# Performance work log

Measured on AMD Instinct MI355X. Metric: run time of the kernel, lower is better.

## Reference

```python
import jax, jax.numpy as jnp
import numpy as np

REG1 = 0.05
REG2 = 0.05

N, D, P = 262144, 256, 512


def setup_inputs() -> dict:
    key = jax.random.key(0)
    kz, kp = jax.random.split(key)
    z = jax.random.normal(kz, (N, D), dtype=jnp.float32)
    # nn.Parameter(torch.rand(P, D)) -> uniform [0, 1)
    prototype_vectors = jax.random.uniform(kp, (P, D), dtype=jnp.float32)
    return {"z": z, "prototype_vectors": prototype_vectors}


def _cdist(a, b):
    # Euclidean pairwise distances [Na, Nb] via the norm trick (matches torch.cdist p=2).
    a2 = jnp.sum(a * a, axis=-1, keepdims=True)          # [Na, 1]
    b2 = jnp.sum(b * b, axis=-1)[None, :]                # [1, Nb]
    sq = a2 + b2 - 2.0 * (a @ b.T)
    return jnp.sqrt(jnp.maximum(sq, 0.0))


def reference(z, prototype_vectors):
    p_dist = _cdist(z, prototype_vectors)                # [N, P]
    f_dist = _cdist(prototype_vectors, z)                # [P, N]
    return (REG1 * jnp.mean(jnp.min(p_dist, axis=1))
            + REG2 * jnp.mean(jnp.min(f_dist, axis=1)))
```

## Files before the change

### kernel.cpp

```cpp
#include <hip/hip_runtime.h>
#include <hip/hip_bf16.h>

#define N_ROWS 262144
#define DDIM   256
#define PROTO  512
#define BM     64
#define RTG    4096
#define NBLK   8192

typedef __bf16 bf16x8 __attribute__((ext_vector_type(8)));
typedef float  f32x4  __attribute__((ext_vector_type(4)));

__global__ void prep_proto(const float* __restrict__ Pm,
                           unsigned short* __restrict__ PBf,
                           float* __restrict__ P2) {
  int p = blockIdx.x;
  int k = threadIdx.x;
  float v = Pm[p * DDIM + k];
  int idx = (p >> 4) * 4096 + (k >> 5) * 512 + ((((k >> 3) & 3) * 16) + (p & 15)) * 8 + (k & 7);
  ((__bf16*)PBf)[idx] = (__bf16)v;
  float sq = v * v;
  #pragma unroll
  for (int m = 1; m < 64; m <<= 1) sq += __shfl_xor(sq, m);
  __shared__ float ws4[4];
  if ((k & 63) == 0) ws4[k >> 6] = sq;
  __syncthreads();
  if (k == 0) P2[p] = (ws4[0] + ws4[1]) + (ws4[2] + ws4[3]);
}

__global__ __launch_bounds__(256, 4)
void proto_main(const float* __restrict__ Z, const unsigned short* __restrict__ PBf,
                const float* __restrict__ P2, float* __restrict__ colpart,
                float* __restrict__ rowminpart) {
  __shared__ __align__(16) unsigned short A_lds[BM * 256];
  __shared__ float z2s[BM];
  __shared__ float rowred[BM * 4];

  const int t   = threadIdx.x;
  const int w   = t >> 6;
  const int l   = t & 63;
  const int l15 = l & 15;
  const int lg  = l >> 4;

  const int bid = blockIdx.x;
  const int g   = ((bid >> 4) << 3) | (bid & 7);
  const int cc  = (bid >> 3) & 1;
  const size_t row0 = (size_t)g * BM;

  const int srow = t >> 2;
  const int sc4  = t & 3;
  {
    const float4* Zv = (const float4*)Z + (row0 + srow) * (DDIM / 4);
    float zacc = 0.f;
    #pragma unroll
    for (int m = 0; m < 8; ++m) {
      float4 a0 = Zv[(sc4 + m * 4) * 2];
      float4 a1 = Zv[(sc4 + m * 4) * 2 + 1];
      zacc += a0.x*a0.x + a0.y*a0.y + a0.z*a0.z + a0.w*a0.w
            + a1.x*a1.x + a1.y*a1.y + a1.z*a1.z + a1.w*a1.w;
      bf16x8 pk;
      pk[0] = (__bf16)a0.x; pk[1] = (__bf16)a0.y; pk[2] = (__bf16)a0.z; pk[3] = (__bf16)a0.w;
      pk[4] = (__bf16)a1.x; pk[5] = (__bf16)a1.y; pk[6] = (__bf16)a1.z; pk[7] = (__bf16)a1.w;
      int slot = (sc4 + m * 4) ^ (srow & 7);
      *(bf16x8*)&A_lds[srow * 256 + slot * 8] = pk;
    }
    zacc += __shfl_xor(zacc, 1);
    zacc += __shfl_xor(zacc, 2);
    if (sc4 == 0) z2s[srow] = zacc;
  }

  float p2r[4];
  #pragma unroll
  for (int j = 0; j < 4; ++j) p2r[j] = P2[cc * 256 + w * 64 + j * 16 + l15];

  __syncthreads();

  f32x4 acc[4][4];
  #pragma unroll
  for (int i = 0; i < 4; ++i)
    #pragma unroll
    for (int j = 0; j < 4; ++j)
      acc[i][j] = (f32x4){0.f, 0.f, 0.f, 0.f};

  const unsigned short* PBw = PBf + (size_t)(cc * 16 + w * 4) * 8 * 512 + l * 8;
  bf16x8 bgn[4];
  #pragma unroll
  for (int j = 0; j < 4; ++j)
    bgn[j] = *(const bf16x8*)&PBw[(size_t)(j * 8) * 512];
  #pragma unroll
  for (int ks = 0; ks < 8; ++ks) {
    bf16x8 bgc[4];
    #pragma unroll
    for (int j = 0; j < 4; ++j) bgc[j] = bgn[j];
    if (ks < 7) {
      #pragma unroll
      for (int j = 0; j < 4; ++j)
        bgn[j] = *(const bf16x8*)&PBw[(size_t)(j * 8 + ks + 1) * 512];
    }
    __builtin_amdgcn_s_setprio(1);
    #pragma unroll
    for (int i = 0; i < 4; ++i) {
      int arow = i * 16 + l15;
      bf16x8 af = *(const bf16x8*)&A_lds[arow * 256 + (((ks * 4 + lg) ^ (l15 & 7)) * 8)];
      #pragma unroll
      for (int j = 0; j < 4; ++j)
        acc[i][j] = __builtin_amdgcn_mfma_f32_16x16x32_bf16(af, bgc[j], acc[i][j], 0, 0, 0);
    }
    __builtin_amdgcn_s_setprio(0);
  }

  float cmin[4] = {3.4e38f, 3.4e38f, 3.4e38f, 3.4e38f};
  #pragma unroll
  for (int i = 0; i < 4; ++i) {
    #pragma unroll
    for (int r = 0; r < 4; ++r) {
      int arow = i * 16 + lg * 4 + r;
      float z2 = z2s[arow];
      float m = 3.4e38f;
      #pragma unroll
      for (int j = 0; j < 4; ++j) {
        float sq = fmaxf(z2 + p2r[j] - 2.0f * acc[i][j][r], 0.0f);
        m = fminf(m, sq);
        cmin[j] = fminf(cmin[j], sq);
      }
      m = fminf(m, __shfl_xor(m, 1));
      m = fminf(m, __shfl_xor(m, 2));
      m = fminf(m, __shfl_xor(m, 4));
      m = fminf(m, __shfl_xor(m, 8));
      if (l15 == 0) rowred[arow * 4 + w] = m;
    }
  }
  #pragma unroll
  for (int j = 0; j < 4; ++j) {
    float c = cmin[j];
    c = fminf(c, __shfl_xor(c, 16));
    c = fminf(c, __shfl_xor(c, 32));
    cmin[j] = c;
  }
  if (l < 16) {
    #pragma unroll
    for (int j = 0; j < 4; ++j)
      colpart[(size_t)g * PROTO + cc * 256 + w * 64 + j * 16 + l] = cmin[j];
  }
  __syncthreads();
  if (t < 64) {
    float m = fminf(fminf(rowred[t * 4], rowred[t * 4 + 1]),
                    fminf(rowred[t * 4 + 2], rowred[t * 4 + 3]));
    rowminpart[(size_t)cc * N_ROWS + row0 + t] = m;
  }
}

__global__ void col_reduce(const float* __restrict__ colpart, float* __restrict__ colfin) {
  int t    = threadIdx.x;
  int colb = blockIdx.x * 16;
  int cl   = t & 15;
  int gg   = t >> 4;
  float m = 3.4e38f;
  for (int g = gg; g < RTG; g += 32)
    m = fminf(m, colpart[(size_t)g * PROTO + colb + cl]);
  m = fminf(m, __shfl_xor(m, 16));
  m = fminf(m, __shfl_xor(m, 32));
  __shared__ float red[8][16];
  if ((t & 63) < 16) red[t >> 6][cl] = m;
  __syncthreads();
  if (t < 16) {
    float r = red[0][t];
    #pragma unroll
    for (int wv = 1; wv < 8; ++wv) r = fminf(r, red[wv][t]);
    colfin[colb + t] = sqrtf(r);
  }
}

__global__ void row_reduce(const float* __restrict__ rowminpart, float* __restrict__ rowsum) {
  int t = threadIdx.x;
  size_t grow = (size_t)blockIdx.x * 256 + t;
  float m = fminf(rowminpart[grow], rowminpart[N_ROWS + grow]);
  float s = sqrtf(m);
  #pragma unroll
  for (int mm = 1; mm < 64; mm <<= 1) s += __shfl_xor(s, mm);
  __shared__ float ws4[4];
  if ((t & 63) == 0) ws4[t >> 6] = s;
  __syncthreads();
  if (t == 0) rowsum[blockIdx.x] = (ws4[0] + ws4[1]) + (ws4[2] + ws4[3]);
}

__global__ void final_reduce(const float* __restrict__ colfin,
                             const float* __restrict__ rowsum,
                             float* __restrict__ out) {
  int t = threadIdx.x;
  float sc = colfin[t];
  float sr = rowsum[t] + rowsum[t + 512];
  #pragma unroll
  for (int mm = 1; mm < 64; mm <<= 1) { sc += __shfl_xor(sc, mm); sr += __shfl_xor(sr, mm); }
  __shared__ float wc[8], wr[8];
  if ((t & 63) == 0) { wc[t >> 6] = sc; wr[t >> 6] = sr; }
  __syncthreads();
  if (t == 0) {
    float tc = 0.f, tr = 0.f;
    #pragma unroll
    for (int i = 0; i < 8; ++i) { tc += wc[i]; tr += wr[i]; }
    out[0] = 0.05f * (tr / (float)N_ROWS) + 0.05f * (tc / (float)PROTO);
  }
}

extern "C" void kernel_launch(void* const* d_in, const int* in_sizes, int n_in,
                              void* d_out, int out_size, void* d_ws, size_t ws_size,
                              hipStream_t stream) {
  const float* z  = (const float*)d_in[0];
  const float* pv = (const float*)d_in[1];
  char* ws = (char*)d_ws;
  size_t off = 0;
  unsigned short* PBf = (unsigned short*)(ws + off); off += 262144;
  float* P2           = (float*)(ws + off);          off += 2048;
  float* colpart      = (float*)(ws + off);          off += (size_t)RTG * PROTO * 4;
  float* colfin       = (float*)(ws + off);          off += 2048;
  float* rowminpart   = (float*)(ws + off);          off += (size_t)2 * N_ROWS * 4;
  float* rowsum       = (float*)(ws + off);          off += 4096;

  prep_proto<<<PROTO, DDIM, 0, stream>>>(pv, PBf, P2);
  proto_main<<<NBLK, 256, 0, stream>>>(z, PBf, P2, colpart, rowminpart);
  col_reduce<<<32, 512, 0, stream>>>(colpart, colfin);
  row_reduce<<<N_ROWS / 256, 256, 0, stream>>>(rowminpart, rowsum);
  final_reduce<<<1, PROTO, 0, stream>>>(colfin, rowsum, (float*)d_out);
}
```

Baseline: 142.2 us.

## Make proto_main persistent over 8 row tiles with double-buffered Z staging

Each block now handles 8 consecutive 64-row tiles instead of one, reducing the grid from 8192 to 1024 blocks. The next tile's Z is prefetched into registers during the current MFMA loop and written to an alternate LDS buffer, and column minima accumulate across tiles. This shrinks the colpart partial array and the col_reduce work. In exchange it doubles LDS use, holds 16 float4 prefetch registers, and lowers the occupancy hint from 4 to 2 blocks per CU.

```diff
diff --git a/kernel.cpp b/kernel.cpp
--- a/kernel.cpp
+++ b/kernel.cpp
@@ -5,8 +5,9 @@
 #define DDIM   256
 #define PROTO  512
 #define BM     64
-#define RTG    4096
-#define NBLK   8192
+#define TPB    8
+#define RGS    512
+#define NBLK   1024
 
 typedef __bf16 bf16x8 __attribute__((ext_vector_type(8)));
 typedef float  f32x4  __attribute__((ext_vector_type(4)));
@@ -28,12 +29,13 @@
   if (k == 0) P2[p] = (ws4[0] + ws4[1]) + (ws4[2] + ws4[3]);
 }
 
-__global__ __launch_bounds__(256, 4)
+__global__ __launch_bounds__(256, 2)
 void proto_main(const float* __restrict__ Z, const unsigned short* __restrict__ PBf,
                 const float* __restrict__ P2, float* __restrict__ colpart,
                 float* __restrict__ rowminpart) {
-  __shared__ __align__(16) unsigned short A_lds[BM * 256];
-  __shared__ float z2s[BM];
+  __shared__ __align__(16) unsigned short A0[BM * 256];
+  __shared__ __align__(16) unsigned short A1[BM * 256];
+  __shared__ float z2s[2][BM];
   __shared__ float rowred[BM * 4];
 
   const int t   = threadIdx.x;
@@ -43,110 +45,145 @@
   const int lg  = l >> 4;
 
   const int bid = blockIdx.x;
-  const int g   = ((bid >> 4) << 3) | (bid & 7);
+  const int rg  = ((bid >> 4) << 3) | (bid & 7);
   const int cc  = (bid >> 3) & 1;
-  const size_t row0 = (size_t)g * BM;
 
   const int srow = t >> 2;
   const int sc4  = t & 3;
+
+  float p2r[4];
+  #pragma unroll
+  for (int j = 0; j < 4; ++j) p2r[j] = P2[cc * 256 + w * 64 + j * 16 + l15];
+
+  float colmin[4] = {3.4e38f, 3.4e38f, 3.4e38f, 3.4e38f};
+
+  const unsigned short* PBw = PBf + (size_t)(cc * 16 + w * 4) * 4096 + l * 8;
+
+  float4 za[16];
   {
-    const float4* Zv = (const float4*)Z + (row0 + srow) * (DDIM / 4);
+    const float4* Zv = (const float4*)Z + ((size_t)rg * TPB * BM + srow) * (DDIM / 4);
+    #pragma unroll
+    for (int m = 0; m < 8; ++m) {
+      za[2 * m]     = Zv[(sc4 + m * 4) * 2];
+      za[2 * m + 1] = Zv[(sc4 + m * 4) * 2 + 1];
+    }
     float zacc = 0.f;
     #pragma unroll
     for (int m = 0; m < 8; ++m) {
-      float4 a0 = Zv[(sc4 + m * 4) * 2];
-      float4 a1 = Zv[(sc4 + m * 4) * 2 + 1];
+      float4 a0 = za[2 * m], a1 = za[2 * m + 1];
       zacc += a0.x*a0.x + a0.y*a0.y + a0.z*a0.z + a0.w*a0.w
             + a1.x*a1.x + a1.y*a1.y + a1.z*a1.z + a1.w*a1.w;
       bf16x8 pk;
       pk[0] = (__bf16)a0.x; pk[1] = (__bf16)a0.y; pk[2] = (__bf16)a0.z; pk[3] = (__bf16)a0.w;
       pk[4] = (__bf16)a1.x; pk[5] = (__bf16)a1.y; pk[6] = (__bf16)a1.z; pk[7] = (__bf16)a1.w;
       int slot = (sc4 + m * 4) ^ (srow & 7);
-      *(bf16x8*)&A_lds[srow * 256 + slot * 8] = pk;
+      *(bf16x8*)&A0[srow * 256 + slot * 8] = pk;
     }
     zacc += __shfl_xor(zacc, 1);
     zacc += __shfl_xor(zacc, 2);
-    if (sc4 == 0) z2s[srow] = zacc;
-  }
-
-  float p2r[4];
-  #pragma unroll
-  for (int j = 0; j < 4; ++j) p2r[j] = P2[cc * 256 + w * 64 + j * 16 + l15];
-
-  __syncthreads();
-
-  f32x4 acc[4][4];
-  #pragma unroll
-  for (int i = 0; i < 4; ++i)
+    if (sc4 == 0) z2s[0][srow] = zacc;
+  }
+  __syncthreads();
+
+  for (int tt = 0; tt < TPB; ++tt) {
+    const int cur = tt & 1;
+    const unsigned short* Ab = cur ? A1 : A0;
+    const size_t row0 = (size_t)(rg * TPB + tt) * BM;
+
+    if (tt < TPB - 1) {
+      const float4* Zv = (const float4*)Z + (row0 + BM + srow) * (DDIM / 4);
+      #pragma unroll
+      for (int m = 0; m < 8; ++m) {
+        za[2 * m]     = Zv[(sc4 + m * 4) * 2];
+        za[2 * m + 1] = Zv[(sc4 + m * 4) * 2 + 1];
+      }
+    }
+
+    f32x4 acc[4][4];
+    #pragma unroll
+    for (int i = 0; i < 4; ++i)
+      #pragma unroll
+      for (int j = 0; j < 4; ++j)
+        acc[i][j] = (f32x4){0.f, 0.f, 0.f, 0.f};
+
+    bf16x8 bgn[4];
     #pragma unroll
     for (int j = 0; j < 4; ++j)
-      acc[i][j] = (f32x4){0.f, 0.f, 0.f, 0.f};
-
-  const unsigned short* PBw = PBf + (size_t)(cc * 16 + w * 4) * 8 * 512 + l * 8;
-  bf16x8 bgn[4];
-  #pragma unroll
-  for (int j = 0; j < 4; ++j)
-    bgn[j] = *(const bf16x8*)&PBw[(size_t)(j * 8) * 512];
-  #pragma unroll
-  for (int ks = 0; ks < 8; ++ks) {
-    bf16x8 bgc[4];
-    #pragma unroll
-    for (int j = 0; j < 4; ++j) bgc[j] = bgn[j];
-    if (ks < 7) {
-      #pragma unroll
-      for (int j = 0; j < 4; ++j)
-        bgn[j] = *(const bf16x8*)&PBw[(size_t)(j * 8 + ks + 1) * 512];
-    }
-    __builtin_amdgcn_s_setprio(1);
+      bgn[j] = *(const bf16x8*)&PBw[(size_t)(j * 8) * 512];
+    #pragma unroll
+    for (int ks = 0; ks < 8; ++ks) {
+      bf16x8 bgc[4];
+      #pragma unroll
+      for (int j = 0; j < 4; ++j) bgc[j] = bgn[j];
+      if (ks < 7) {
+        #pragma unroll
+        for (int j = 0; j < 4; ++j)
+          bgn[j] = *(const bf16x8*)&PBw[(size_t)(j * 8 + ks + 1) * 512];
+      }
+      __builtin_amdgcn_s_setprio(1);
+      #pragma unroll
+      for (int i = 0; i < 4; ++i) {
+        bf16x8 af = *(const bf16x8*)&Ab[(i * 16 + l15) * 256 + (((ks * 4 + lg) ^ (l15 & 7)) * 8)];
+        #pragma unroll
+        for (int j = 0; j < 4; ++j)
+          acc[i][j] = __builtin_amdgcn_mfma_f32_16x16x32_bf16(af, bgc[j], acc[i][j], 0, 0, 0);
+      }
+      __builtin_amdgcn_s_setprio(0);
+    }
+
     #pragma unroll
     for (int i = 0; i < 4; ++i) {
-      int arow = i * 16 + l15;
-      bf16x8 af = *(const bf16x8*)&A_lds[arow * 256 + (((ks * 4 + lg) ^ (l15 & 7)) * 8)];
-      #pragma unroll
-      for (int j = 0; j < 4; ++j)
-        acc[i][j] = __builtin_amdgcn_mfma_f32_16x16x32_bf16(af, bgc[j], acc[i][j], 0, 0, 0);
-    }
-    __builtin_amdgcn_s_setprio(0);
-  }
-
-  float cmin[4] = {3.4e38f, 3.4e38f, 3.4e38f, 3.4e38f};
-  #pragma unroll
-  for (int i = 0; i < 4; ++i) {
-    #pragma unroll
-    for (int r = 0; r < 4; ++r) {
-      int arow = i * 16 + lg * 4 + r;
-      float z2 = z2s[arow];
-      float m = 3.4e38f;
-      #pragma unroll
-      for (int j = 0; j < 4; ++j) {
-        float sq = fmaxf(z2 + p2r[j] - 2.0f * acc[i][j][r], 0.0f);
-        m = fminf(m, sq);
-        cmin[j] = fminf(cmin[j], sq);
-      }
-      m = fminf(m, __shfl_xor(m, 1));
-      m = fminf(m, __shfl_xor(m, 2));
-      m = fminf(m, __shfl_xor(m, 4));
-      m = fminf(m, __shfl_xor(m, 8));
-      if (l15 == 0) rowred[arow * 4 + w] = m;
-    }
-  }
-  #pragma unroll
-  for (int j = 0; j < 4; ++j) {
-    float c = cmin[j];
-    c = fminf(c, __shfl_xor(c, 16));
-    c = fminf(c, __shfl_xor(c, 32));
-    cmin[j] = c;
-  }
+      #pragma unroll
+      for (int r = 0; r < 4; ++r) {
+        int arow = i * 16 + lg * 4 + r;
+        float z2 = z2s[cur][arow];
+        float m = 3.4e38f;
+        #pragma unroll
+        for (int j = 0; j < 4; ++j) {
+          float sq = fmaxf(z2 + p2r[j] - 2.0f * acc[i][j][r], 0.0f);
+          m = fminf(m, sq);
+          colmin[j] = fminf(colmin[j], sq);
+        }
+        m = fminf(m, __shfl_xor(m, 1));
+        m = fminf(m, __shfl_xor(m, 2));
+        m = fminf(m, __shfl_xor(m, 4));
+        m = fminf(m, __shfl_xor(m, 8));
+        if (l15 == 0) rowred[arow * 4 + w] = m;
+      }
+    }
+    __syncthreads();
+
+    if (t < 64) {
+      float m = fminf(fminf(rowred[t * 4], rowred[t * 4 + 1]),
+                      fminf(rowred[t * 4 + 2], rowred[t * 4 + 3]));
+      rowminpart[(size_t)cc * N_ROWS + row0 + t] = m;
+    }
+
+    if (tt < TPB - 1) {
+      unsigned short* An = cur ? A0 : A1;
+      float zacc = 0.f;
+      #pragma unroll
+      for (int m = 0; m < 8; ++m) {
+        float4 a0 = za[2 * m], a1 = za[2 * m + 1];
+        zacc += a0.x*a0.x + a0.y*a0.y + a0.z*a0.z + a0.w*a0.w
+              + a1.x*a1.x + a1.y*a1.y + a1.z*a1.z + a1.w*a1.w;
+        bf16x8 pk;
+        pk[0] = (__bf16)a0.x; pk[1] = (__bf16)a0.y; pk[2] = (__bf16)a0.z; pk[3] = (__bf16)a0.w;
+        pk[4] = (__bf16)a1.x; pk[5] = (__bf16)a1.y; pk[6] = (__bf16)a1.z; pk[7] = (__bf16)a1.w;
+        int slot = (sc4 + m * 4) ^ (srow & 7);
+        *(bf16x8*)&An[srow * 256 + slot * 8] = pk;
+      }
+      zacc += __shfl_xor(zacc, 1);
+      zacc += __shfl_xor(zacc, 2);
+      if (sc4 == 0) z2s[cur ^ 1][srow] = zacc;
+    }
+    __syncthreads();
+  }
+
   if (l < 16) {
     #pragma unroll
     for (int j = 0; j < 4; ++j)
-      colpart[(size_t)g * PROTO + cc * 256 + w * 64 + j * 16 + l] = cmin[j];
-  }
-  __syncthreads();
-  if (t < 64) {
-    float m = fminf(fminf(rowred[t * 4], rowred[t * 4 + 1]),
-                    fminf(rowred[t * 4 + 2], rowred[t * 4 + 3]));
-    rowminpart[(size_t)cc * N_ROWS + row0 + t] = m;
+      colpart[(size_t)rg * PROTO + cc * 256 + w * 64 + j * 16 + l] = colmin[j];
   }
 }
 
@@ -156,7 +193,7 @@
   int cl   = t & 15;
   int gg   = t >> 4;
   float m = 3.4e38f;
-  for (int g = gg; g < RTG; g += 32)
+  for (int g = gg; g < RGS; g += 32)
     m = fminf(m, colpart[(size_t)g * PROTO + colb + cl]);
   m = fminf(m, __shfl_xor(m, 16));
   m = fminf(m, __shfl_xor(m, 32));
@@ -212,7 +249,7 @@
   size_t off = 0;
   unsigned short* PBf = (unsigned short*)(ws + off); off += 262144;
   float* P2           = (float*)(ws + off);          off += 2048;
-  float* colpart      = (float*)(ws + off);          off += (size_t)RTG * PROTO * 4;
+  float* colpart      = (float*)(ws + off);          off += (size_t)RGS * PROTO * 4;
   float* colfin       = (float*)(ws + off);          off += 2048;
   float* rowminpart   = (float*)(ws + off);          off += (size_t)2 * N_ROWS * 4;
   float* rowsum       = (float*)(ws + off);          off += 4096;
```

After: 487.1 us. 3.43x slower.
